# Kernel optimization log

Hardware: AMD Instinct MI355X
Metric: run time of the kernel (lower is better)

Reference implementation:

```python
import jax, jax.numpy as jnp
import numpy as np

N_NODES = 100000
N_EDGES = 1600000


def _degrees(idx, n_nodes):
    # degree per node, clamped to >=1 (DGL GraphConv norm='both' behavior)
    d = jax.ops.segment_sum(jnp.ones(idx.shape[0], jnp.float32), idx, num_segments=n_nodes)
    return jnp.maximum(d, 1.0)


def _graph_conv(x, src, dst, W, b, n_nodes, activation=False):
    # DGL GraphConv, norm='both': h = D_in^{-1/2} A (D_out^{-1/2} X W) + b
    # in_feats >= out_feats, so weight is applied before aggregation.
    out_norm = _degrees(src, n_nodes) ** -0.5  # [N]
    in_norm = _degrees(dst, n_nodes) ** -0.5   # [N]
    h = (x * out_norm[:, None]) @ W            # [N, out]
    agg = jax.ops.segment_sum(h[src], dst, num_segments=n_nodes)  # SpMM gather-scatter
    h = agg * in_norm[:, None] + b
    return jax.nn.relu(h) if activation else h


def setup_inputs() -> dict:
    key = jax.random.key(0)
    ks = jax.random.split(key, 6)
    in_size, hid_size, out_size = 64, 64, 32
    features = jax.random.normal(ks[0], (N_NODES, in_size), jnp.float32)
    src = jax.random.randint(ks[1], (N_EDGES,), 0, N_NODES, jnp.int32)
    dst = jax.random.randint(ks[2], (N_EDGES,), 0, N_NODES, jnp.int32)
    # Glorot-style init scale
    W1 = jax.random.normal(ks[3], (in_size, hid_size), jnp.float32) * (1.0 / np.sqrt(in_size))
    b1 = jnp.zeros((hid_size,), jnp.float32)
    W2 = jax.random.normal(ks[4], (hid_size, out_size), jnp.float32) * (1.0 / np.sqrt(hid_size))
    b2 = jnp.zeros((out_size,), jnp.float32)
    return {"features": features, "src": src, "dst": dst, "W1": W1, "b1": b1, "W2": W2, "b2": b2}


def reference(features, src, dst, W1, b1, W2, b2):
    # Layer 1: GraphConv + ReLU. Dropout (p=0.5) is identity in eval mode.
    h = _graph_conv(features, src, dst, W1, b1, N_NODES, activation=True)
    # Layer 2: GraphConv (no activation)
    return _graph_conv(h, src, dst, W2, b2, N_NODES, activation=False)
```

## Files before the change

kernel.cpp:

```cpp
#include <hip/hip_runtime.h>
#include <hip/hip_fp16.h>


#define BIN_SH 8
#define NBINS 391
#define SRC_OFF 512
#define CAP 5120
#define KB_EPT 8

__global__ __launch_bounds__(1024) void kBx(
    const int* __restrict__ src, const int* __restrict__ dst,
    int* __restrict__ gcur, int* __restrict__ binbuf_d,
    unsigned char* __restrict__ binbuf_s,
    const float* __restrict__ x, const float* __restrict__ W,
    __half* __restrict__ h1, int E, int n, int NKB, int GX) {
  __shared__ __align__(16) char smem[53248];
  int bid = blockIdx.x;
  int Mn = (NKB < GX) ? NKB : GX;
  bool isKB;
  int idx;
  if (bid < 2 * Mn) { isKB = !(bid & 1); idx = bid >> 1; }
  else               { isKB = (NKB > GX); idx = bid - 2 * Mn + Mn; }

  int t = threadIdx.x;
  if (isKB) {
    int* stage_d = (int*)smem;
    unsigned char* stage_s = (unsigned char*)(smem + 32768);
    int* cnt_d  = (int*)(smem + 40960);
    int* cnt_s  = (int*)(smem + 43008);
    int* scan_d = (int*)(smem + 45056);
    int* scan_s = (int*)(smem + 47104);
    int* base_d = (int*)(smem + 49152);
    int* base_s = (int*)(smem + 51200);

    if (t < 512) { cnt_d[t] = 0; cnt_s[t] = 0; }
    __syncthreads();
    int base = idx * (1024 * KB_EPT);
#pragma unroll
    for (int i = 0; i < KB_EPT; i++) {
      int e = base + i * 1024 + t;
      if (e < E) {
        atomicAdd(&cnt_d[dst[e] >> BIN_SH], 1);
        atomicAdd(&cnt_s[src[e] >> BIN_SH], 1);
      }
    }
    __syncthreads();
    {
      int* tmp = stage_d;
      int v = (t < 512) ? cnt_d[t] : cnt_s[t - 512];
      tmp[t] = v;
      __syncthreads();
#pragma unroll
      for (int off = 1; off < 512; off <<= 1) {
        int val = ((t & 511) >= off) ? tmp[t - off] : 0;
        __syncthreads();
        tmp[t] += val;
        __syncthreads();
      }
      int ex = tmp[t] - v;
      if (t < 512) scan_d[t] = ex; else scan_s[t - 512] = ex;
      __syncthreads();
    }
    if (t < 512) {
      int c = cnt_d[t];
      base_d[t] = c ? atomicAdd(&gcur[t], c) : 0;
    } else {
      int i = t - 512;
      int cs = cnt_s[i];
      base_s[i] = cs ? atomicAdd(&gcur[SRC_OFF + i], cs) : 0;
    }
    __syncthreads();
    if (t < 512) { cnt_d[t] = 0; cnt_s[t] = 0; }
    __syncthreads();
#pragma unroll
    for (int i = 0; i < KB_EPT; i++) {
      int e = base + i * 1024 + t;
      if (e < E) {
        int d = dst[e], s = src[e];
        int bd = d >> BIN_SH;
        int rd = atomicAdd(&cnt_d[bd], 1);
        stage_d[scan_d[bd] + rd] = ((d & 255) << 17) | s;
        int bs = s >> BIN_SH;
        int rs = atomicAdd(&cnt_s[bs], 1);
        stage_s[scan_s[bs] + rs] = (unsigned char)(s & 255);
      }
    }
    __syncthreads();
    int wv = t >> 6, ln = t & 63;
    for (int b = wv; b < NBINS; b += 16) {
      int sd = scan_d[b], cd = scan_d[b + 1] - sd;
      int gd = b * CAP + base_d[b];
      for (int j = ln; j < cd; j += 64) binbuf_d[gd + j] = stage_d[sd + j];
      int ss = scan_s[b], cs = scan_s[b + 1] - ss;
      int gs = b * CAP + base_s[b];
      for (int j = ln; j < cs; j += 64) binbuf_s[gs + j] = stage_s[ss + j];
    }
    return;
  }
  float* Ws = (float*)smem;
  float* xs = Ws + 64 * 64;
#pragma unroll
  for (int i = 0; i < 4; i++) Ws[i * 1024 + t] = W[i * 1024 + t];
  int row0 = idx * 64;
  {
    int r = t >> 4, k4 = t & 15;
    int row = row0 + r;
    float4 v = make_float4(0.f, 0.f, 0.f, 0.f);
    if (row < n) v = ((const float4*)x)[(size_t)row * 16 + k4];
    ((float4*)xs)[t] = v;
  }
  __syncthreads();
  int c = t & 63, rq = t >> 6;
  float acc[4] = {0.f, 0.f, 0.f, 0.f};
#pragma unroll 4
  for (int kq = 0; kq < 16; kq++) {
    float w0 = Ws[(4 * kq + 0) * 64 + c];
    float w1 = Ws[(4 * kq + 1) * 64 + c];
    float w2 = Ws[(4 * kq + 2) * 64 + c];
    float w3 = Ws[(4 * kq + 3) * 64 + c];
#pragma unroll
    for (int rr = 0; rr < 4; rr++) {
      const float4 xv = *(const float4*)&xs[(rq + rr * 16) * 64 + kq * 4];
      acc[rr] += xv.x * w0 + xv.y * w1 + xv.z * w2 + xv.w * w3;
    }
  }
#pragma unroll
  for (int rr = 0; rr < 4; rr++) {
    int row = row0 + rq + rr * 16;
    if (row < n) h1[(size_t)row * 64 + c] = __float2half(acc[rr]);
  }
}

__global__ __launch_bounds__(1024) void kC_build(
    const int* __restrict__ gcur, const int* __restrict__ binbuf_d,
    const unsigned char* __restrict__ binbuf_s,
    int* __restrict__ col, int* __restrict__ rowptr, int* __restrict__ deg,
    float* __restrict__ in_norm, float* __restrict__ out_norm,
    __half* __restrict__ h1, int n) {
  __shared__ int lcnt[256];
  __shared__ int lptr[256];
  __shared__ int red[1024];
  int b = blockIdx.x;
  int t = threadIdx.x;
  if (b >= NBINS) {
    int sb = b - NBINS;
    int cnt = gcur[SRC_OFF + sb];
    const unsigned int* p4 =
        (const unsigned int*)(binbuf_s + (size_t)sb * CAP);
    if (t < 256) lcnt[t] = 0;
    __syncthreads();
    int cw = (cnt + 3) >> 2;
    for (int i = t; i < cw; i += 1024) {
      unsigned int v = p4[i];
      int rem = cnt - i * 4;
      atomicAdd(&lcnt[v & 255], 1);
      if (rem > 1) atomicAdd(&lcnt[(v >> 8) & 255], 1);
      if (rem > 2) atomicAdd(&lcnt[(v >> 16) & 255], 1);
      if (rem > 3) atomicAdd(&lcnt[v >> 24], 1);
    }
    __syncthreads();
    int node0 = sb << BIN_SH;
    float* onn = (float*)lptr;
    if (t < 256) {
      float o = rsqrtf(fmaxf((float)lcnt[t], 1.0f));
      if (node0 + t < n) out_norm[node0 + t] = o;
      onn[t] = o;
    }
    __syncthreads();
    uint4* h1q = (uint4*)h1 + (size_t)node0 * 8;
#pragma unroll
    for (int i = 0; i < 2; i++) {
      int idx = i * 1024 + t;
      int r = idx >> 3;
      if (node0 + r < n) {
        float sc = onn[r];
        uint4 v = h1q[idx];
        __half2* hp = (__half2*)&v;
#pragma unroll
        for (int q = 0; q < 4; q++) {
          float2 f = __half22float2(hp[q]);
          f.x *= sc; f.y *= sc;
          hp[q] = __float22half2_rn(f);
        }
        h1q[idx] = v;
      }
    }
    return;
  }
  int cnt = gcur[b];
  const int* items = binbuf_d + (size_t)b * CAP;
  if (t < 256) lcnt[t] = 0;
  __syncthreads();
  for (int i = t; i < cnt; i += 1024) atomicAdd(&lcnt[items[i] >> 17], 1);
  red[t] = (t < b) ? gcur[t] : 0;
  __syncthreads();
#pragma unroll
  for (int off = 512; off > 0; off >>= 1) {
    if (t < off) red[t] += red[t + off];
    __syncthreads();
  }
  int ebase = red[0];
  int cv = 0;
  if (t < 256) { cv = lcnt[t]; lptr[t] = cv; }
  __syncthreads();
#pragma unroll
  for (int off = 1; off < 256; off <<= 1) {
    int val = (t < 256 && t >= off) ? lptr[t - off] : 0;
    __syncthreads();
    if (t < 256) lptr[t] += val;
    __syncthreads();
  }
  if (t < 256) {
    int ex = lptr[t] - cv;
    int node = (b << BIN_SH) + t;
    if (node < n) {
      rowptr[node] = ebase + ex;
      deg[node] = cv;
      in_norm[node] = rsqrtf(fmaxf((float)cv, 1.0f));
    }
    lptr[t] = ex;
  }
  __syncthreads();
  for (int i = t; i < cnt; i += 1024) {
    int v = items[i];
    int r = atomicAdd(&lptr[v >> 17], 1);
    col[ebase + r] = v & 0x1FFFF;
  }
}

__device__ inline void add8h(float* a, uint4 r) {
  const __half2* hp = reinterpret_cast<const __half2*>(&r);
#pragma unroll
  for (int i = 0; i < 4; i++) {
    float2 f = __half22float2(hp[i]);
    a[2 * i] += f.x;
    a[2 * i + 1] += f.y;
  }
}

__global__ __launch_bounds__(256) void pull64_xw2(
    const int* __restrict__ rowptr, const int* __restrict__ deg,
    const int* __restrict__ col, const __half* __restrict__ h1,
    const float* __restrict__ out_norm, const float* __restrict__ in_norm,
    const float* __restrict__ b1, const float* __restrict__ W2,
    __half* __restrict__ h2, int n) {
  __shared__ float W2s[64 * 32];
  __shared__ float xrow[32][64];
  int t = threadIdx.x;
#pragma unroll
  for (int i = 0; i < 8; i++) W2s[i * 256 + t] = W2[i * 256 + t];

  int w = t >> 6, l = t & 63, g = l >> 3, fq = l & 7;
  int r = w * 8 + g;
  int node = blockIdx.x * 32 + r;

  if (node < n) {
    int beg = rowptr[node];
    int dg = deg[node];
    float a0[8] = {0, 0, 0, 0, 0, 0, 0, 0};
    float a1[8] = {0, 0, 0, 0, 0, 0, 0, 0};
    int i = 0;
    for (; i + 4 <= dg; i += 4) {
      int s0 = col[beg + i];
      int s1 = col[beg + i + 1];
      int s2 = col[beg + i + 2];
      int s3 = col[beg + i + 3];
      uint4 v0 = ((const uint4*)h1)[(size_t)s0 * 8 + fq];
      uint4 v1 = ((const uint4*)h1)[(size_t)s1 * 8 + fq];
      uint4 v2 = ((const uint4*)h1)[(size_t)s2 * 8 + fq];
      uint4 v3 = ((const uint4*)h1)[(size_t)s3 * 8 + fq];
      add8h(a0, v0);
      add8h(a1, v1);
      add8h(a0, v2);
      add8h(a1, v3);
    }
    for (; i < dg; i++) {
      int s = col[beg + i];
      uint4 v = ((const uint4*)h1)[(size_t)s * 8 + fq];
      add8h(a0, v);
    }
    float innv = in_norm[node];
    float onnv = out_norm[node];
    float4 ba = ((const float4*)b1)[fq * 2];
    float4 bb = ((const float4*)b1)[fq * 2 + 1];
    float4 o0, o1;
    o0.x = fmaxf((a0[0] + a1[0]) * innv + ba.x, 0.0f) * onnv;
    o0.y = fmaxf((a0[1] + a1[1]) * innv + ba.y, 0.0f) * onnv;
    o0.z = fmaxf((a0[2] + a1[2]) * innv + ba.z, 0.0f) * onnv;
    o0.w = fmaxf((a0[3] + a1[3]) * innv + ba.w, 0.0f) * onnv;
    o1.x = fmaxf((a0[4] + a1[4]) * innv + bb.x, 0.0f) * onnv;
    o1.y = fmaxf((a0[5] + a1[5]) * innv + bb.y, 0.0f) * onnv;
    o1.z = fmaxf((a0[6] + a1[6]) * innv + bb.z, 0.0f) * onnv;
    o1.w = fmaxf((a0[7] + a1[7]) * innv + bb.w, 0.0f) * onnv;
    *(float4*)&xrow[r][fq * 8] = o0;
    *(float4*)&xrow[r][fq * 8 + 4] = o1;
  }
  __syncthreads();
  int c = t & 31, nq = t >> 5;
#pragma unroll
  for (int p = 0; p < 4; p++) {
    int rr = p * 8 + nq;
    int nd = blockIdx.x * 32 + rr;
    if (nd < n) {
      float dot = 0.f;
#pragma unroll 16
      for (int k = 0; k < 64; k++) dot += xrow[rr][k] * W2s[k * 32 + c];
      h2[(size_t)nd * 32 + c] = __float2half(dot);
    }
  }
}

__global__ __launch_bounds__(256) void gcn_pull32(const int* __restrict__ rowptr,
                                                  const int* __restrict__ deg,
                                                  const int* __restrict__ col,
                                                  const __half* __restrict__ h,
                                                  const float* __restrict__ in_norm,
                                                  const float* __restrict__ b2,
                                                  float* __restrict__ out, int n) {
  int t = threadIdx.x;
  int w = t >> 6, l = t & 63, g = l >> 2, fq = l & 3;
  int node = blockIdx.x * 64 + w * 16 + g;
  if (node >= n) return;
  int beg = rowptr[node];
  int dg = deg[node];
  float a0[8] = {0, 0, 0, 0, 0, 0, 0, 0};
  float a1[8] = {0, 0, 0, 0, 0, 0, 0, 0};
  int i = 0;
  for (; i + 4 <= dg; i += 4) {
    int s0 = col[beg + i];
    int s1 = col[beg + i + 1];
    int s2 = col[beg + i + 2];
    int s3 = col[beg + i + 3];
    uint4 v0 = ((const uint4*)h)[(size_t)s0 * 4 + fq];
    uint4 v1 = ((const uint4*)h)[(size_t)s1 * 4 + fq];
    uint4 v2 = ((const uint4*)h)[(size_t)s2 * 4 + fq];
    uint4 v3 = ((const uint4*)h)[(size_t)s3 * 4 + fq];
    add8h(a0, v0);
    add8h(a1, v1);
    add8h(a0, v2);
    add8h(a1, v3);
  }
  for (; i < dg; i++) {
    int s = col[beg + i];
    uint4 v = ((const uint4*)h)[(size_t)s * 4 + fq];
    add8h(a0, v);
  }
  float innv = in_norm[node];
  float4 b2a = ((const float4*)b2)[fq * 2];
  float4 b2b = ((const float4*)b2)[fq * 2 + 1];
  float4 o0, o1;
  o0.x = (a0[0] + a1[0]) * innv + b2a.x;
  o0.y = (a0[1] + a1[1]) * innv + b2a.y;
  o0.z = (a0[2] + a1[2]) * innv + b2a.z;
  o0.w = (a0[3] + a1[3]) * innv + b2a.w;
  o1.x = (a0[4] + a1[4]) * innv + b2b.x;
  o1.y = (a0[5] + a1[5]) * innv + b2b.y;
  o1.z = (a0[6] + a1[6]) * innv + b2b.z;
  o1.w = (a0[7] + a1[7]) * innv + b2b.w;
  ((float4*)out)[(size_t)node * 8 + fq * 2] = o0;
  ((float4*)out)[(size_t)node * 8 + fq * 2 + 1] = o1;
}

extern "C" void kernel_launch(void* const* d_in, const int* in_sizes, int n_in,
                              void* d_out, int out_size, void* d_ws, size_t ws_size,
                              hipStream_t stream) {
  const float* x   = (const float*)d_in[0];
  const int*   src = (const int*)d_in[1];
  const int*   dst = (const int*)d_in[2];
  const float* W1  = (const float*)d_in[3];
  const float* b1  = (const float*)d_in[4];
  const float* W2  = (const float*)d_in[5];
  const float* b2  = (const float*)d_in[6];
  float* out = (float*)d_out;

  const int N = in_sizes[0] / 64;
  const int E = in_sizes[1];

  int* deg        = (int*)d_ws;
  int* rowptr     = deg + N;
  float* in_norm  = (float*)(rowptr + N);
  float* out_norm = in_norm + N;
  int* gcur       = (int*)(out_norm + N);
  int* col        = gcur + 1024;
  __half* h1 = (__half*)(col + E);
  __half* h2 = h1 + (size_t)64 * N;
  int* binbuf_d = (int*)h2;
  unsigned char* binbuf_s =
      (unsigned char*)(binbuf_d + (size_t)NBINS * CAP);

  hipMemsetAsync(gcur, 0, 1024 * sizeof(int), stream);

  const int NKB = (E + 1024 * KB_EPT - 1) / (1024 * KB_EPT);
  const int GX = (N + 63) / 64;
  kBx<<<NKB + GX, 1024, 0, stream>>>(src, dst, gcur, binbuf_d, binbuf_s,
                                     x, W1, h1, E, N, NKB, GX);
  kC_build<<<2 * NBINS, 1024, 0, stream>>>(gcur, binbuf_d, binbuf_s, col, rowptr,
                                           deg, in_norm, out_norm, h1, N);
  pull64_xw2<<<(N + 31) / 32, 256, 0, stream>>>(rowptr, deg, col, h1, out_norm,
                                                in_norm, b1, W2, h2, N);
  gcn_pull32<<<(N + 63) / 64, 256, 0, stream>>>(rowptr, deg, col, h2, in_norm,
                                                b2, out, N);
}
```

Before: 204.2 us.

## Sort nodes by degree within each bin to balance pull-kernel wavefronts

The CSR build kernel now counting-sorts each 256-node bin by in-degree (capped at 63) and writes a permuted node index array. Both pull kernels read node ids through this index, so threads in a wavefront handle nodes of similar degree and loop divergence drops. The cost is an extra indirection load, scattered output writes, and a little more work plus synchronisation in the build kernel.

```diff
diff --git a/kernel.cpp b/kernel.cpp
--- a/kernel.cpp
+++ b/kernel.cpp
@@ -136,7 +136,7 @@
     const unsigned char* __restrict__ binbuf_s,
     int* __restrict__ col, int* __restrict__ rowptr, int* __restrict__ deg,
     float* __restrict__ in_norm, float* __restrict__ out_norm,
-    __half* __restrict__ h1, int n) {
+    __half* __restrict__ h1, int* __restrict__ sidx, int n) {
   __shared__ int lcnt[256];
   __shared__ int lptr[256];
   __shared__ int red[1024];
@@ -226,6 +226,23 @@
     int r = atomicAdd(&lptr[v >> 17], 1);
     col[ebase + r] = v & 0x1FFFF;
   }
+  __syncthreads();
+  if (t < 64) red[t] = 0;
+  if (t < 256) sidx[(b << BIN_SH) + t] = -1;
+  __syncthreads();
+  int bkt = 0, myrank = 0;
+  bool valid = (t < 256) && (((b << BIN_SH) + t) < n);
+  if (valid) {
+    bkt = cv < 63 ? cv : 63;
+    myrank = atomicAdd(&red[bkt], 1);
+  }
+  __syncthreads();
+  if (t == 0) {
+    int s = 0;
+    for (int i2 = 0; i2 < 64; i2++) { int c2 = red[i2]; red[64 + i2] = s; s += c2; }
+  }
+  __syncthreads();
+  if (valid) sidx[(b << BIN_SH) + red[64 + bkt] + myrank] = (b << BIN_SH) + t;
 }
 
 __device__ inline void add8h(float* a, uint4 r) {
@@ -243,18 +260,20 @@
     const int* __restrict__ col, const __half* __restrict__ h1,
     const float* __restrict__ out_norm, const float* __restrict__ in_norm,
     const float* __restrict__ b1, const float* __restrict__ W2,
-    __half* __restrict__ h2, int n) {
+    const int* __restrict__ sidx, __half* __restrict__ h2, int n) {
   __shared__ float W2s[64 * 32];
   __shared__ float xrow[32][64];
+  __shared__ int nodebuf[32];
   int t = threadIdx.x;
 #pragma unroll
   for (int i = 0; i < 8; i++) W2s[i * 256 + t] = W2[i * 256 + t];
 
   int w = t >> 6, l = t & 63, g = l >> 3, fq = l & 7;
   int r = w * 8 + g;
-  int node = blockIdx.x * 32 + r;
-
-  if (node < n) {
+  int node = sidx[blockIdx.x * 32 + r];
+  nodebuf[r] = node;
+
+  if (node >= 0) {
     int beg = rowptr[node];
     int dg = deg[node];
     float a0[8] = {0, 0, 0, 0, 0, 0, 0, 0};
@@ -300,8 +319,8 @@
 #pragma unroll
   for (int p = 0; p < 4; p++) {
     int rr = p * 8 + nq;
-    int nd = blockIdx.x * 32 + rr;
-    if (nd < n) {
+    int nd = nodebuf[rr];
+    if (nd >= 0) {
       float dot = 0.f;
 #pragma unroll 16
       for (int k = 0; k < 64; k++) dot += xrow[rr][k] * W2s[k * 32 + c];
@@ -316,11 +335,12 @@
                                                   const __half* __restrict__ h,
                                                   const float* __restrict__ in_norm,
                                                   const float* __restrict__ b2,
+                                                  const int* __restrict__ sidx,
                                                   float* __restrict__ out, int n) {
   int t = threadIdx.x;
   int w = t >> 6, l = t & 63, g = l >> 2, fq = l & 3;
-  int node = blockIdx.x * 64 + w * 16 + g;
-  if (node >= n) return;
+  int node = sidx[blockIdx.x * 64 + w * 16 + g];
+  if (node < 0) return;
   int beg = rowptr[node];
   int dg = deg[node];
   float a0[8] = {0, 0, 0, 0, 0, 0, 0, 0};
@@ -375,13 +395,15 @@
 
   const int N = in_sizes[0] / 64;
   const int E = in_sizes[1];
+  const int NSLOT = NBINS * 256;
 
   int* deg        = (int*)d_ws;
   int* rowptr     = deg + N;
   float* in_norm  = (float*)(rowptr + N);
   float* out_norm = in_norm + N;
   int* gcur       = (int*)(out_norm + N);
-  int* col        = gcur + 1024;
+  int* sidx       = gcur + 1024;
+  int* col        = sidx + NSLOT;
   __half* h1 = (__half*)(col + E);
   __half* h2 = h1 + (size_t)64 * N;
   int* binbuf_d = (int*)h2;
@@ -395,9 +417,9 @@
   kBx<<<NKB + GX, 1024, 0, stream>>>(src, dst, gcur, binbuf_d, binbuf_s,
                                      x, W1, h1, E, N, NKB, GX);
   kC_build<<<2 * NBINS, 1024, 0, stream>>>(gcur, binbuf_d, binbuf_s, col, rowptr,
-                                           deg, in_norm, out_norm, h1, N);
-  pull64_xw2<<<(N + 31) / 32, 256, 0, stream>>>(rowptr, deg, col, h1, out_norm,
-                                                in_norm, b1, W2, h2, N);
-  gcn_pull32<<<(N + 63) / 64, 256, 0, stream>>>(rowptr, deg, col, h2, in_norm,
-                                                b2, out, N);
-}
+                                           deg, in_norm, out_norm, h1, sidx, N);
+  pull64_xw2<<<NBINS * 8, 256, 0, stream>>>(rowptr, deg, col, h1, out_norm,
+                                            in_norm, b1, W2, sidx, h2, N);
+  gcn_pull32<<<NBINS * 4, 256, 0, stream>>>(rowptr, deg, col, h2, in_norm,
+                                            b2, sidx, out, N);
+}
```

Result: slower. 220.0 us (+7.7%).
